# Performance work log

Hardware: AMD Instinct MI355X
Metric: run time of the kernel (lower is better)

## Reference

```python
import jax, jax.numpy as jnp
import numpy as np

DMODEL = 1024
H = 16
DK = DMODEL // H  # 64
B, L = 4, 4096


def setup_inputs() -> dict:
    key = jax.random.key(0)
    ks = jax.random.split(key, 9)
    Q = jax.random.normal(ks[0], (B, L, DMODEL), dtype=jnp.float32)
    K = jax.random.normal(ks[1], (B, L, DMODEL), dtype=jnp.float32)
    V = jax.random.normal(ks[2], (B, L, DMODEL), dtype=jnp.float32)
    s = 1.0 / np.sqrt(DMODEL)
    Wq = jax.random.normal(ks[3], (DMODEL, DK), dtype=jnp.float32) * s
    Wk = jax.random.normal(ks[4], (DMODEL, DK), dtype=jnp.float32) * s
    Wv = jax.random.normal(ks[5], (DMODEL, DK), dtype=jnp.float32) * s
    bq = jnp.zeros((DK,), jnp.float32)
    bk = jnp.zeros((DK,), jnp.float32)
    bv = jnp.zeros((DK,), jnp.float32)
    # causal self-attention mask: True where attention is DISALLOWED (masked_fill semantics)
    causal = ~jnp.tril(jnp.ones((L, L), dtype=bool))  # [L, L]
    mask_self_attention = jnp.broadcast_to(causal, (B, L, L))
    return {"Q": Q, "K": K, "V": V, "Wq": Wq, "bq": bq, "Wk": Wk, "bk": bk,
            "Wv": Wv, "bv": bv, "mask_self_attention": mask_self_attention}


def reference(Q, K, V, Wq, bq, Wk, bk, Wv, bv, mask_self_attention):
    # per-head linear projections: [B, L, dmodel] -> [B, L, dk]
    q = jnp.einsum('bld,dk->blk', Q, Wq) + bq
    k = jnp.einsum('bld,dk->blk', K, Wk) + bk
    v = jnp.einsum('bld,dk->blk', V, Wv) + bv
    # scores: [B, L, L]
    scores = jnp.einsum('blk,bmk->blm', q, k) / jnp.sqrt(jnp.float32(DK))
    scores = jnp.where(mask_self_attention, -jnp.inf, scores)
    attn = jax.nn.softmax(scores, axis=-1)
    # dropout_rate = 0.0 -> identity
    return jnp.einsum('blm,bmk->blk', attn, v)
```

## Files before the change

### kernel.cpp

```cpp
#include <hip/hip_runtime.h>
#include <hip/hip_bf16.h>
#include <math.h>

#define DM 1024
#define DKx 64
#define NB 4
#define LL 4096
#define MTOT (NB * LL)

#define CHUNK 8
#define NCH 8

typedef __attribute__((ext_vector_type(8))) __bf16 bf16x8;
typedef __attribute__((ext_vector_type(4))) __bf16 bf16x4;
typedef __attribute__((ext_vector_type(4))) float f32x4;

#define SCALE_LOG2E 0.18033688011112042f

__device__ __forceinline__ f32x4 mfma16(bf16x8 a, bf16x8 b, f32x4 c) {
  return __builtin_amdgcn_mfma_f32_16x16x32_bf16(a, b, c, 0, 0, 0);
}

extern "C" __global__ __launch_bounds__(256) void prep_kernel(
    const float* __restrict__ Wq, const float* __restrict__ Wk, const float* __restrict__ Wv,
    const float* __restrict__ bq, const float* __restrict__ bk, const float* __restrict__ bv,
    __bf16* __restrict__ Wt, float* __restrict__ bsf)
{
  const int which = blockIdx.y;
  const float* W    = (which == 0) ? Wq : (which == 1) ? Wk : Wv;
  const float* bsrc = (which == 0) ? bq : (which == 1) ? bk : bv;
  const float scale = (which == 0) ? SCALE_LOG2E : 1.f;

  const int tid  = threadIdx.x;
  const int lane = tid & 63;
  const int n    = blockIdx.x * 4 + (tid >> 6);

  __bf16* dst = Wt + ((size_t)which * 64 + n) * DM;
#pragma unroll
  for (int i = 0; i < 2; ++i) {
    const int k0 = lane * 16 + i * 8;
    bf16x8 v;
#pragma unroll
    for (int j = 0; j < 8; ++j)
      v[j] = (__bf16)(W[(size_t)(k0 + j) * DKx + n] * scale);
    *reinterpret_cast<bf16x8*>(dst + k0) = v;
  }
  if (blockIdx.x == 0 && tid < 64) bsf[which * 64 + tid] = bsrc[tid] * scale;
}

extern "C" __global__ __launch_bounds__(256) void proj_kernel(
    const float* __restrict__ Xq, const float* __restrict__ Xk, const float* __restrict__ Xv,
    const __bf16* __restrict__ Wt, const float* __restrict__ bsf,
    __bf16* __restrict__ qo, __bf16* __restrict__ ko, __bf16* __restrict__ vTo)
{
  const int which = blockIdx.y;
  const float* X = (which == 0) ? Xq : (which == 1) ? Xk : Xv;
  const __bf16* Wrow = Wt + (size_t)which * 64 * DM;
  const float* bias  = bsf + which * 64;

  const int tid  = threadIdx.x;
  const int wave = tid >> 6;
  const int lane = tid & 63;
  const int quad = lane >> 4;
  const int c    = lane & 15;
  const int rowbase = blockIdx.x * 64;
  const int arow = rowbase + wave * 16 + c;

  f32x4 acc[4];
#pragma unroll
  for (int t = 0; t < 4; ++t) acc[t] = (f32x4){0.f, 0.f, 0.f, 0.f};

#pragma unroll 2
  for (int kk = 0; kk < DM; kk += 64) {
    bf16x8 af[2];
#pragma unroll
    for (int s = 0; s < 2; ++s) {
      const float* src = X + (size_t)arow * DM + kk + s * 32 + quad * 8;
      float4 u0 = *reinterpret_cast<const float4*>(src);
      float4 u1 = *reinterpret_cast<const float4*>(src + 4);
      bf16x8 a;
      a[0] = (__bf16)u0.x; a[1] = (__bf16)u0.y; a[2] = (__bf16)u0.z; a[3] = (__bf16)u0.w;
      a[4] = (__bf16)u1.x; a[5] = (__bf16)u1.y; a[6] = (__bf16)u1.z; a[7] = (__bf16)u1.w;
      af[s] = a;
    }
#pragma unroll
    for (int t = 0; t < 4; ++t) {
      const __bf16* wp = Wrow + (size_t)(t * 16 + c) * DM + kk + quad * 8;
      bf16x8 b0 = *reinterpret_cast<const bf16x8*>(wp);
      bf16x8 b1 = *reinterpret_cast<const bf16x8*>(wp + 32);
      acc[t] = mfma16(af[0], b0, acc[t]);
      acc[t] = mfma16(af[1], b1, acc[t]);
    }
  }

#pragma unroll
  for (int t = 0; t < 4; ++t) {
    const int col = t * 16 + c;
    const float bb = bias[col];
#pragma unroll
    for (int r = 0; r < 4; ++r) {
      const float v = acc[t][r] + bb;
      const int row = rowbase + wave * 16 + quad * 4 + r;
      const __bf16 h = (__bf16)v;
      if (which == 0)      qo[(size_t)row * DKx + col] = h;
      else if (which == 1) ko[(size_t)row * DKx + col] = h;
      else                 vTo[((size_t)(row >> 12) * DKx + col) * LL + (row & (LL - 1))] = h;
    }
  }
}

extern "C" __global__ __launch_bounds__(256, 4) void attn_kernel(
    const __bf16* __restrict__ qws, const __bf16* __restrict__ kws,
    const __bf16* __restrict__ vTws, float* __restrict__ Opart,
    float* __restrict__ mpart, float* __restrict__ lpart)
{
  const int tile = blockIdx.x;
  const int b    = blockIdx.y;
  const int s_ch = blockIdx.z;
  if (s_ch * CHUNK > tile) return;
  const int jbeg = s_ch * CHUNK;
  const int jend = min(tile + 1, jbeg + CHUNK);

  const int tid  = threadIdx.x;
  const int wave = tid >> 6;
  const int lane = tid & 63;
  const int quad = lane >> 4;
  const int c    = lane & 15;
  const int qbase = tile * 64;

  __shared__ __bf16 sK[64 * 72];
  __shared__ __bf16 sVt[64 * 72];
  __shared__ __bf16 sP[64 * 72];

  bf16x8 qf[2];
  {
    const __bf16* qp = qws + (size_t)(b * LL + qbase + wave * 16 + c) * DKx + quad * 8;
    qf[0] = *reinterpret_cast<const bf16x8*>(qp);
    qf[1] = *reinterpret_cast<const bf16x8*>(qp + 32);
  }

  f32x4 o[4];
#pragma unroll
  for (int t = 0; t < 4; ++t) o[t] = (f32x4){0.f, 0.f, 0.f, 0.f};
  float m_[4], l_[4];
#pragma unroll
  for (int r = 0; r < 4; ++r) { m_[r] = -1e30f; l_[r] = 0.f; }

  const int rr0 = tid >> 3;
  const int seg = tid & 7;

  for (int j = jbeg; j < jend; ++j) {
    const int n0 = j * 64;
    __syncthreads();
    {
      const __bf16* kp = kws + (size_t)(b * LL + n0 + rr0) * DKx + seg * 8;
      *reinterpret_cast<bf16x8*>(&sK[rr0 * 72 + seg * 8]) =
          *reinterpret_cast<const bf16x8*>(kp);
      *reinterpret_cast<bf16x8*>(&sK[(rr0 + 32) * 72 + seg * 8]) =
          *reinterpret_cast<const bf16x8*>(kp + 32 * DKx);
      const __bf16* vp = vTws + (size_t)(b * DKx + rr0) * LL + n0 + seg * 8;
      *reinterpret_cast<bf16x8*>(&sVt[rr0 * 72 + seg * 8]) =
          *reinterpret_cast<const bf16x8*>(vp);
      *reinterpret_cast<bf16x8*>(&sVt[(rr0 + 32) * 72 + seg * 8]) =
          *reinterpret_cast<const bf16x8*>(vp + (size_t)32 * LL);
    }
    __syncthreads();

    f32x4 s[4];
#pragma unroll
    for (int t = 0; t < 4; ++t) {
      bf16x8 b0 = *reinterpret_cast<const bf16x8*>(&sK[(t * 16 + c) * 72 + quad * 8]);
      bf16x8 b1 = *reinterpret_cast<const bf16x8*>(&sK[(t * 16 + c) * 72 + 32 + quad * 8]);
      f32x4 z = (f32x4){0.f, 0.f, 0.f, 0.f};
      z = mfma16(qf[0], b0, z);
      s[t] = mfma16(qf[1], b1, z);
    }

    if (j == tile) {
#pragma unroll
      for (int t = 0; t < 4; ++t)
#pragma unroll
        for (int r = 0; r < 4; ++r)
          if (t * 16 + c > wave * 16 + quad * 4 + r) s[t][r] = -1e30f;
    }

    float mc[4], alpha[4], psum[4];
#pragma unroll
    for (int r = 0; r < 4; ++r)
      mc[r] = fmaxf(fmaxf(s[0][r], s[1][r]), fmaxf(s[2][r], s[3][r]));
#pragma unroll
    for (int r = 0; r < 4; ++r) {
      mc[r] = fmaxf(mc[r], __shfl_xor(mc[r], 1));
      mc[r] = fmaxf(mc[r], __shfl_xor(mc[r], 2));
      mc[r] = fmaxf(mc[r], __shfl_xor(mc[r], 4));
      mc[r] = fmaxf(mc[r], __shfl_xor(mc[r], 8));
    }
#pragma unroll
    for (int r = 0; r < 4; ++r) {
      const float mn = fmaxf(m_[r], mc[r]);
      alpha[r] = __builtin_amdgcn_exp2f(m_[r] - mn);
      m_[r] = mn;
      psum[r] = 0.f;
    }
#pragma unroll
    for (int t = 0; t < 4; ++t)
#pragma unroll
      for (int r = 0; r < 4; ++r) {
        const float p = __builtin_amdgcn_exp2f(s[t][r] - m_[r]);
        s[t][r] = p;
        psum[r] += p;
      }
#pragma unroll
    for (int r = 0; r < 4; ++r) {
      psum[r] += __shfl_xor(psum[r], 1);
      psum[r] += __shfl_xor(psum[r], 2);
      psum[r] += __shfl_xor(psum[r], 4);
      psum[r] += __shfl_xor(psum[r], 8);
      l_[r] = l_[r] * alpha[r] + psum[r];
    }

#pragma unroll
    for (int t = 0; t < 4; ++t)
#pragma unroll
      for (int r = 0; r < 4; ++r) {
        sP[(wave * 16 + quad * 4 + r) * 72 + t * 16 + c] = (__bf16)s[t][r];
        o[t][r] *= alpha[r];
      }

    bf16x8 pf0 = *reinterpret_cast<const bf16x8*>(&sP[(wave * 16 + c) * 72 + quad * 8]);
    bf16x8 pf1 = *reinterpret_cast<const bf16x8*>(&sP[(wave * 16 + c) * 72 + 32 + quad * 8]);
#pragma unroll
    for (int t = 0; t < 4; ++t) {
      bf16x8 v0 = *reinterpret_cast<const bf16x8*>(&sVt[(t * 16 + c) * 72 + quad * 8]);
      bf16x8 v1 = *reinterpret_cast<const bf16x8*>(&sVt[(t * 16 + c) * 72 + 32 + quad * 8]);
      o[t] = mfma16(pf0, v0, o[t]);
      o[t] = mfma16(pf1, v1, o[t]);
    }
  }

  float* Op = Opart + (((size_t)(b * 64 + tile) * NCH + s_ch) * 64 * 64);
#pragma unroll
  for (int r = 0; r < 4; ++r) {
    const int rl = wave * 16 + quad * 4 + r;
#pragma unroll
    for (int t = 0; t < 4; ++t)
      Op[rl * 64 + t * 16 + c] = o[t][r];
    if (c == 0) {
      const size_t mi = ((size_t)(b * 64 + tile) * NCH + s_ch) * 64 + rl;
      mpart[mi] = m_[r];
      lpart[mi] = l_[r];
    }
  }
}

extern "C" __global__ __launch_bounds__(256) void combine_kernel(
    const float* __restrict__ Opart, const float* __restrict__ mpart,
    const float* __restrict__ lpart, float* __restrict__ out)
{
  const int tile = blockIdx.x;
  const int b    = blockIdx.y;
  const int nch  = tile / CHUNK + 1;
  const int tid  = threadIdx.x;
  const int row  = tid >> 2;
  const int cg   = tid & 3;
  const size_t base = (size_t)(b * 64 + tile) * NCH;

  float m = -1e30f;
  for (int s = 0; s < nch; ++s)
    m = fmaxf(m, mpart[(base + s) * 64 + row]);
  float denom = 0.f;
  for (int s = 0; s < nch; ++s)
    denom += __builtin_amdgcn_exp2f(mpart[(base + s) * 64 + row] - m) *
             lpart[(base + s) * 64 + row];
  const float inv = 1.f / denom;

  f32x4 acc[4];
#pragma unroll
  for (int i = 0; i < 4; ++i) acc[i] = (f32x4){0.f, 0.f, 0.f, 0.f};
  for (int s = 0; s < nch; ++s) {
    const float w = __builtin_amdgcn_exp2f(mpart[(base + s) * 64 + row] - m);
    const f32x4* op = reinterpret_cast<const f32x4*>(
        Opart + (base + s) * 64 * 64 + row * 64 + cg * 16);
#pragma unroll
    for (int i = 0; i < 4; ++i) {
      f32x4 v = op[i];
#pragma unroll
      for (int e = 0; e < 4; ++e) acc[i][e] += w * v[e];
    }
  }
  float* dst = out + (size_t)(b * LL + tile * 64 + row) * DKx + cg * 16;
#pragma unroll
  for (int i = 0; i < 4; ++i) {
    f32x4 v;
#pragma unroll
    for (int e = 0; e < 4; ++e) v[e] = acc[i][e] * inv;
    reinterpret_cast<f32x4*>(dst)[i] = v;
  }
}

extern "C" void kernel_launch(void* const* d_in, const int* in_sizes, int n_in,
                              void* d_out, int out_size, void* d_ws, size_t ws_size,
                              hipStream_t stream)
{
  const float* Q  = (const float*)d_in[0];
  const float* K  = (const float*)d_in[1];
  const float* V  = (const float*)d_in[2];
  const float* Wq = (const float*)d_in[3];
  const float* bq = (const float*)d_in[4];
  const float* Wk = (const float*)d_in[5];
  const float* bk = (const float*)d_in[6];
  const float* Wv = (const float*)d_in[7];
  const float* bv = (const float*)d_in[8];
  float* out = (float*)d_out;

  __bf16* qws = (__bf16*)d_ws;
  __bf16* kws = qws + (size_t)MTOT * DKx;
  __bf16* vT  = kws + (size_t)MTOT * DKx;
  float* Opart = (float*)(vT + (size_t)MTOT * DKx);
  float* mpart = Opart + (size_t)NB * 64 * NCH * 64 * 64;
  float* lpart = mpart + (size_t)NB * 64 * NCH * 64;
  __bf16* Wt   = (__bf16*)(lpart + (size_t)NB * 64 * NCH * 64);
  float* bsf   = (float*)(Wt + (size_t)3 * 64 * DM);

  prep_kernel<<<dim3(16, 3), 256, 0, stream>>>(Wq, Wk, Wv, bq, bk, bv, Wt, bsf);
  proj_kernel<<<dim3(MTOT / 64, 3), 256, 0, stream>>>(
      Q, K, V, Wt, bsf, qws, kws, vT);
  attn_kernel<<<dim3(LL / 64, NB, NCH), 256, 0, stream>>>(
      qws, kws, vT, Opart, mpart, lpart);
  combine_kernel<<<dim3(LL / 64, NB), 256, 0, stream>>>(Opart, mpart, lpart, out);
}
```

Measured before the change: 506.6 us.

## Stage projection weights in LDS with double buffering and coalesce output stores

The projection kernel now copies each 64x128 slice of the transposed bf16 weight into a double-buffered shared-memory tile, so all four waves share one global read instead of each fetching it separately. The K loop is unrolled to 128-wide steps with four MFMAs per output tile. The epilogue stages results through shared memory so q/k rows and the transposed v are written with 16-byte vector stores instead of scattered 2-byte stores, which matters most for the strided vT layout. This adds LDS usage and barriers per iteration, which may lower occupancy.

```diff
diff --git a/kernel.cpp b/kernel.cpp
--- a/kernel.cpp
+++ b/kernel.cpp
@@ -57,6 +57,8 @@
   const float* X = (which == 0) ? Xq : (which == 1) ? Xk : Xv;
   const __bf16* Wrow = Wt + (size_t)which * 64 * DM;
   const float* bias  = bsf + which * 64;
+
+  __shared__ __bf16 sW[2][64 * 136];
 
   const int tid  = threadIdx.x;
   const int wave = tid >> 6;
@@ -66,15 +68,29 @@
   const int rowbase = blockIdx.x * 64;
   const int arow = rowbase + wave * 16 + c;
 
+  const int sn = tid & 63;
+  const int sh = tid >> 6;
+
   f32x4 acc[4];
 #pragma unroll
   for (int t = 0; t < 4; ++t) acc[t] = (f32x4){0.f, 0.f, 0.f, 0.f};
 
-#pragma unroll 2
-  for (int kk = 0; kk < DM; kk += 64) {
-    bf16x8 af[2];
-#pragma unroll
-    for (int s = 0; s < 2; ++s) {
+  {
+    const __bf16* src = Wrow + (size_t)sn * DM + sh * 32;
+    __bf16* dst = &sW[0][sn * 136 + sh * 32];
+#pragma unroll
+    for (int p = 0; p < 4; ++p)
+      *reinterpret_cast<bf16x8*>(dst + p * 8) =
+          *reinterpret_cast<const bf16x8*>(src + p * 8);
+  }
+  __syncthreads();
+
+#pragma unroll
+  for (int i = 0; i < 8; ++i) {
+    const int kk = i * 128;
+    bf16x8 af[4];
+#pragma unroll
+    for (int s = 0; s < 4; ++s) {
       const float* src = X + (size_t)arow * DM + kk + s * 32 + quad * 8;
       float4 u0 = *reinterpret_cast<const float4*>(src);
       float4 u1 = *reinterpret_cast<const float4*>(src + 4);
@@ -83,29 +99,58 @@
       a[4] = (__bf16)u1.x; a[5] = (__bf16)u1.y; a[6] = (__bf16)u1.z; a[7] = (__bf16)u1.w;
       af[s] = a;
     }
-#pragma unroll
-    for (int t = 0; t < 4; ++t) {
-      const __bf16* wp = Wrow + (size_t)(t * 16 + c) * DM + kk + quad * 8;
-      bf16x8 b0 = *reinterpret_cast<const bf16x8*>(wp);
-      bf16x8 b1 = *reinterpret_cast<const bf16x8*>(wp + 32);
-      acc[t] = mfma16(af[0], b0, acc[t]);
-      acc[t] = mfma16(af[1], b1, acc[t]);
-    }
-  }
-
-#pragma unroll
-  for (int t = 0; t < 4; ++t) {
-    const int col = t * 16 + c;
-    const float bb = bias[col];
-#pragma unroll
-    for (int r = 0; r < 4; ++r) {
-      const float v = acc[t][r] + bb;
-      const int row = rowbase + wave * 16 + quad * 4 + r;
-      const __bf16 h = (__bf16)v;
-      if (which == 0)      qo[(size_t)row * DKx + col] = h;
-      else if (which == 1) ko[(size_t)row * DKx + col] = h;
-      else                 vTo[((size_t)(row >> 12) * DKx + col) * LL + (row & (LL - 1))] = h;
-    }
+    if (i < 7) {
+      const __bf16* src = Wrow + (size_t)sn * DM + kk + 128 + sh * 32;
+      __bf16* dst = &sW[(i + 1) & 1][sn * 136 + sh * 32];
+#pragma unroll
+      for (int p = 0; p < 4; ++p)
+        *reinterpret_cast<bf16x8*>(dst + p * 8) =
+            *reinterpret_cast<const bf16x8*>(src + p * 8);
+    }
+    const __bf16* wb = &sW[i & 1][0];
+#pragma unroll
+    for (int t = 0; t < 4; ++t) {
+      const __bf16* wp = wb + (t * 16 + c) * 136 + quad * 8;
+#pragma unroll
+      for (int s = 0; s < 4; ++s)
+        acc[t] = mfma16(af[s], *reinterpret_cast<const bf16x8*>(wp + s * 32), acc[t]);
+    }
+    __syncthreads();
+  }
+
+  __bf16* sT = &sW[0][0];
+  if (which == 2) {
+#pragma unroll
+    for (int t = 0; t < 4; ++t) {
+      const float bb = bias[t * 16 + c];
+#pragma unroll
+      for (int r = 0; r < 4; ++r)
+        sT[(t * 16 + c) * 72 + wave * 16 + quad * 4 + r] = (__bf16)(acc[t][r] + bb);
+    }
+  } else {
+#pragma unroll
+    for (int t = 0; t < 4; ++t) {
+      const float bb = bias[t * 16 + c];
+#pragma unroll
+      for (int r = 0; r < 4; ++r)
+        sT[(wave * 16 + quad * 4 + r) * 72 + t * 16 + c] = (__bf16)(acc[t][r] + bb);
+    }
+  }
+  __syncthreads();
+  if (which == 2) {
+    const int col  = tid >> 2;
+    const int rseg = (tid & 3) * 16;
+    __bf16* dst = vTo + ((size_t)(rowbase >> 12) * DKx + col) * LL +
+                  (rowbase & (LL - 1)) + rseg;
+    *reinterpret_cast<bf16x8*>(dst)     = *reinterpret_cast<bf16x8*>(&sT[col * 72 + rseg]);
+    *reinterpret_cast<bf16x8*>(dst + 8) = *reinterpret_cast<bf16x8*>(&sT[col * 72 + rseg + 8]);
+  } else {
+    const int rl   = tid >> 2;
+    const int cseg = (tid & 3) * 16;
+    __bf16* o = (which == 0) ? qo : ko;
+    __bf16* dst = o + (size_t)(rowbase + rl) * DKx + cseg;
+    *reinterpret_cast<bf16x8*>(dst)     = *reinterpret_cast<bf16x8*>(&sT[rl * 72 + cseg]);
+    *reinterpret_cast<bf16x8*>(dst + 8) = *reinterpret_cast<bf16x8*>(&sT[rl * 72 + cseg + 8]);
   }
 }
 
```

Result: faster. 489.1 us (-3.5%).
